# Performance work log

Hardware: AMD Instinct MI355X
Metric: run time of the kernel (lower is better)

The kernel has to match this reference:

```python
import jax, jax.numpy as jnp
import numpy as np

EMB_DIM = 256
Q_DIM = 512
V_DIM = 512

def setup_inputs() -> dict:
    key = jax.random.key(0)
    ks = jax.random.split(key, 7)
    B, S = 8, 2048
    x = jax.random.normal(ks[0], (B, S, EMB_DIM), dtype=jnp.float32)
    s = 1.0 / np.sqrt(EMB_DIM)
    Wq = jax.random.normal(ks[1], (EMB_DIM, Q_DIM), dtype=jnp.float32) * s
    bq = jax.random.normal(ks[2], (Q_DIM,), dtype=jnp.float32) * 0.01
    Wk = jax.random.normal(ks[3], (EMB_DIM, Q_DIM), dtype=jnp.float32) * s
    bk = jax.random.normal(ks[4], (Q_DIM,), dtype=jnp.float32) * 0.01
    Wv = jax.random.normal(ks[5], (EMB_DIM, V_DIM), dtype=jnp.float32) * s
    bv = jax.random.normal(ks[6], (V_DIM,), dtype=jnp.float32) * 0.01
    return {"x": x, "Wq": Wq, "bq": bq, "Wk": Wk, "bk": bk, "Wv": Wv, "bv": bv}

def reference(x, Wq, bq, Wk, bk, Wv, bv):
    # q/k/v projections (torch Linear == x @ W + b with W stored [in, out] here)
    q = jax.nn.sigmoid(jnp.einsum('bse,eq->bsq', x, Wq) + bq)   # [B,S,Q]
    k = jnp.einsum('bse,eq->bsq', x, Wk) + bk                   # [B,S,Q]
    v = jnp.einsum('bse,ev->bsv', x, Wv) + bv                   # [B,S,V]
    scale = 1.0 / jnp.sqrt(jnp.float32(EMB_DIM))
    qk = jnp.einsum('bsq,btq->bst', q, k) * scale               # [B,S,S]
    qk = jax.nn.elu(qk)
    attn = jax.nn.softmax(qk, axis=-1)
    return jnp.einsum('bst,btv->bsv', attn, v)                  # [B,S,V]
```

## Files before the change

kernel.cpp:

```cpp
#include <hip/hip_runtime.h>
#include <hip/hip_bf16.h>
#include <math.h>

typedef unsigned short u16;
using short8 = __attribute__((ext_vector_type(8))) short;
using f32x4  = __attribute__((ext_vector_type(4))) float;

#define BK 32


__device__ __forceinline__ u16 f2bf(float f) {
  union { float f; unsigned u; } v; v.f = f;
  unsigned r = v.u + 0x7FFFu + ((v.u >> 16) & 1u);
  return (u16)(r >> 16);
}

__device__ __forceinline__ float fexp(float x) { return __expf(x); }

__device__ __forceinline__ void gld16(const void* g, void* l) {
  __builtin_amdgcn_global_load_lds(
      (const __attribute__((address_space(1))) void*)g,
      (__attribute__((address_space(3))) void*)l,
      16, 0, 0);
}


__device__ __forceinline__ void gemm_core64(const u16* __restrict__ Ag,
                                            const u16* __restrict__ Bg,
                                            int K, int lda, int ldb,
                                            u16* As, u16* Bs,
                                            f32x4 acc[4][4], int w, int l) {
  const int wm = (w & 1) << 6, wn = (w >> 1) << 6;
  const int ln = l & 15, lq = l >> 4;
  const int sr0 = w * 16 + (l >> 2);
  const int sr1 = 64 + sr0;
  const int skp = (l & 3) * 8;
  const int skg = ((l & 3) ^ ((l >> 3) & 3)) * 8;
  const int kro = (lq ^ ((ln >> 1) & 3)) * 8;

#pragma unroll
  for (int mt = 0; mt < 4; mt++)
#pragma unroll
    for (int nt = 0; nt < 4; nt++) acc[mt][nt] = (f32x4)0.0f;

  for (int k0 = 0; k0 < K; k0 += 64) {
    __syncthreads();
    gld16(Ag + (size_t)sr0 * lda + k0 + skg, As + sr0 * BK + skp);
    gld16(Ag + (size_t)sr1 * lda + k0 + skg, As + sr1 * BK + skp);
    gld16(Ag + (size_t)sr0 * lda + k0 + 32 + skg, As + 4096 + sr0 * BK + skp);
    gld16(Ag + (size_t)sr1 * lda + k0 + 32 + skg, As + 4096 + sr1 * BK + skp);
    gld16(Bg + (size_t)sr0 * ldb + k0 + skg, Bs + sr0 * BK + skp);
    gld16(Bg + (size_t)sr1 * ldb + k0 + skg, Bs + sr1 * BK + skp);
    gld16(Bg + (size_t)sr0 * ldb + k0 + 32 + skg, Bs + 4096 + sr0 * BK + skp);
    gld16(Bg + (size_t)sr1 * ldb + k0 + 32 + skg, Bs + 4096 + sr1 * BK + skp);
    __syncthreads();
#pragma unroll
    for (int h = 0; h < 2; h++) {
      const u16* Ah = As + h * 4096;
      const u16* Bh = Bs + h * 4096;
      short8 af[4], bf[4];
#pragma unroll
      for (int mt = 0; mt < 4; mt++)
        af[mt] = *(const short8*)(Ah + (wm + mt * 16 + ln) * BK + kro);
#pragma unroll
      for (int nt = 0; nt < 4; nt++)
        bf[nt] = *(const short8*)(Bh + (wn + nt * 16 + ln) * BK + kro);
#pragma unroll
      for (int mt = 0; mt < 4; mt++)
#pragma unroll
        for (int nt = 0; nt < 4; nt++)
          acc[mt][nt] = __builtin_amdgcn_mfma_f32_16x16x32_bf16(
              af[mt], bf[nt], acc[mt][nt], 0, 0, 0);
    }
  }
}


__global__ __launch_bounds__(256) void k_conv(
    const float* __restrict__ x, u16* __restrict__ xb,
    const float* __restrict__ Wq, const float* __restrict__ Wk,
    const float* __restrict__ Wv, const float* __restrict__ bq,
    const float* __restrict__ bk, const float* __restrict__ bv,
    u16* __restrict__ Wt, float* __restrict__ bcat,
    float* __restrict__ lsum) {
  const int bid = blockIdx.x;
  if (bid < 4096) {
    int i = bid * 256 + threadIdx.x;
    float4 v = ((const float4*)x)[i];
    ushort4 o;
    o.x = f2bf(v.x); o.y = f2bf(v.y); o.z = f2bf(v.z); o.w = f2bf(v.w);
    ((ushort4*)xb)[i] = o;
  } else if (bid < 5632) {
    int i = (bid - 4096) * 256 + threadIdx.x;
    int nn = i >> 8, e = i & 255;
    int sel = nn >> 9, c = nn & 511;
    const float* W = (sel == 0) ? Wq : (sel == 1) ? Wk : Wv;
    Wt[i] = f2bf(W[e * 512 + c]);
    if (e == 0) {
      const float* bb = (sel == 0) ? bq : (sel == 1) ? bk : bv;
      bcat[nn] = bb[c];
    }
  } else {
    int i = (bid - 5632) * 256 + threadIdx.x;
    lsum[i] = 0.0f;
  }
}


__global__ __launch_bounds__(256) void k_proj(
    const u16* __restrict__ xb, const u16* __restrict__ Wt,
    const float* __restrict__ bcat, u16* __restrict__ qb,
    u16* __restrict__ kb, u16* __restrict__ vtb) {
  __shared__ __align__(16) u16 As8[8 * 4096];
  __shared__ __align__(16) u16 Bs[2 * 4096];
  const int bm = blockIdx.y * 128;
  const int bnq = blockIdx.x;
  const int tid = threadIdx.x, w = tid >> 6, l = tid & 63;
  const int wm = (w & 1) << 6, wn = (w >> 1) << 6;
  const int ln = l & 15, lq = l >> 4;
  const int sr0 = w * 16 + (l >> 2);
  const int sr1 = 64 + sr0;
  const int skp = (l & 3) * 8;
  const int skg = ((l & 3) ^ ((l >> 3) & 3)) * 8;
  const int kro = (lq ^ ((ln >> 1) & 3)) * 8;

#pragma unroll
  for (int kw = 0; kw < 8; kw++) {
    gld16(xb + (size_t)(bm + sr0) * 256 + kw * 32 + skg,
          As8 + kw * 4096 + sr0 * BK + skp);
    gld16(xb + (size_t)(bm + sr1) * 256 + kw * 32 + skg,
          As8 + kw * 4096 + sr1 * BK + skp);
  }

  const int b = bm >> 11, t0 = bm & 2047;
  const int cb = bnq * 128;

  for (int p = 0; p < 3; p++) {
    const u16* Bg = Wt + (size_t)(p * 512 + cb) * 256;
    f32x4 acc[4][4];
#pragma unroll
    for (int mt = 0; mt < 4; mt++)
#pragma unroll
      for (int nt = 0; nt < 4; nt++) acc[mt][nt] = (f32x4)0.0f;

#pragma unroll
    for (int it2 = 0; it2 < 4; it2++) {
      __syncthreads();
      gld16(Bg + (size_t)sr0 * 256 + it2 * 64 + skg, Bs + sr0 * BK + skp);
      gld16(Bg + (size_t)sr1 * 256 + it2 * 64 + skg, Bs + sr1 * BK + skp);
      gld16(Bg + (size_t)sr0 * 256 + it2 * 64 + 32 + skg,
            Bs + 4096 + sr0 * BK + skp);
      gld16(Bg + (size_t)sr1 * 256 + it2 * 64 + 32 + skg,
            Bs + 4096 + sr1 * BK + skp);
      __syncthreads();
#pragma unroll
      for (int h = 0; h < 2; h++) {
        const u16* Aw = As8 + (it2 * 2 + h) * 4096;
        const u16* Bh = Bs + h * 4096;
        short8 af[4], bf[4];
#pragma unroll
        for (int mt = 0; mt < 4; mt++)
          af[mt] = *(const short8*)(Aw + (wm + mt * 16 + ln) * BK + kro);
#pragma unroll
        for (int nt = 0; nt < 4; nt++)
          bf[nt] = *(const short8*)(Bh + (wn + nt * 16 + ln) * BK + kro);
#pragma unroll
        for (int mt = 0; mt < 4; mt++)
#pragma unroll
          for (int nt = 0; nt < 4; nt++)
            acc[mt][nt] = __builtin_amdgcn_mfma_f32_16x16x32_bf16(
                af[mt], bf[nt], acc[mt][nt], 0, 0, 0);
      }
    }

    if (p < 2) {
      u16* dst = p ? kb : qb;
#pragma unroll
      for (int mt = 0; mt < 4; mt++)
#pragma unroll
        for (int r = 0; r < 4; r++) {
          int row = bm + wm + mt * 16 + lq * 4 + r;
#pragma unroll
          for (int nt = 0; nt < 4; nt++) {
            int col = wn + nt * 16 + ln;
            float v = acc[mt][nt][r] + bcat[p * 512 + cb + col];
            float ov = (p == 0) ? __builtin_amdgcn_rcpf(1.0f + fexp(-v)) : v;
            dst[(size_t)row * 512 + cb + col] = f2bf(ov);
          }
        }
    } else {
      u16* tr = As8;
#pragma unroll
      for (int h = 0; h < 2; h++) {
        __syncthreads();
        if ((w & 1) == h) {
#pragma unroll
          for (int mt = 0; mt < 4; mt++)
#pragma unroll
            for (int nt = 0; nt < 4; nt++) {
              int c = wn + nt * 16 + ln;
              float bias = bcat[1024 + cb + c];
#pragma unroll
              for (int r = 0; r < 4; r++) {
                int lr = mt * 16 + lq * 4 + r;
                tr[c * 68 + lr] = f2bf(acc[mt][nt][r] + bias);
              }
            }
        }
        __syncthreads();
        int c2 = tid >> 1, half = tid & 1;
        size_t dbase = ((size_t)b * 512 + cb + c2) * 2048 + t0 + h * 64 + half * 32;
#pragma unroll
        for (int j = 0; j < 4; j++) {
          ushort4 a0 = *(const ushort4*)&tr[c2 * 68 + half * 32 + j * 8];
          ushort4 a1 = *(const ushort4*)&tr[c2 * 68 + half * 32 + j * 8 + 4];
          *(ushort4*)&vtb[dbase + j * 8] = a0;
          *(ushort4*)&vtb[dbase + j * 8 + 4] = a1;
        }
      }
    }
  }
}


__global__ __launch_bounds__(256, 4) void k_qk(const u16* __restrict__ qb,
                                               const u16* __restrict__ kb,
                                               u16* __restrict__ P,
                                               float* __restrict__ lsum) {
  __shared__ __align__(16) u16 As[2 * 4096];
  __shared__ __align__(16) u16 Bs[2 * 4096];
  const int bid = blockIdx.x;
  const int b = bid & 7, t = bid >> 3;
  const int bm = (t >> 4) * 128, bn = (t & 15) * 128;
  const size_t ob = (size_t)b * 2048 * 512;
  const int tid = threadIdx.x, w = tid >> 6, l = tid & 63;
  f32x4 acc[4][4];
  gemm_core64(qb + ob + (size_t)bm * 512, kb + ob + (size_t)bn * 512,
              512, 512, 512, As, Bs, acc, w, l);

  const int wm = (w & 1) << 6, wn = (w >> 1) << 6;
  const int ln = l & 15, lq = l >> 4;
  const float scale = 0.0625f;
#pragma unroll
  for (int mt = 0; mt < 4; mt++)
#pragma unroll
    for (int r = 0; r < 4; r++) {
      int row = bm + wm + mt * 16 + lq * 4 + r;
      float s = 0.0f;
#pragma unroll
      for (int nt = 0; nt < 4; nt++) {
        int col = bn + wn + nt * 16 + ln;
        float v = acc[mt][nt][r] * scale;
        float e = (v > 0.0f) ? v : (fexp(v) - 1.0f);
        float p = fexp(e);
        P[((size_t)b * 2048 + row) * 2048 + col] = f2bf(p);
        s += p;
      }
#pragma unroll
      for (int o = 1; o < 16; o <<= 1) s += __shfl_xor(s, o);
      if (ln == 0) atomicAdd(&lsum[b * 2048 + row], s);
    }
}


__global__ __launch_bounds__(256, 4) void k_pv(const u16* __restrict__ P,
                                               const u16* __restrict__ vtb,
                                               const float* __restrict__ lsum,
                                               float* __restrict__ out) {
  __shared__ __align__(16) u16 As[2 * 4096];
  __shared__ __align__(16) u16 Bs[2 * 4096];
  const int bid = blockIdx.x;
  const int b = bid & 7, t = bid >> 3;
  const int bm = (t >> 2) * 128, bn = (t & 3) * 128;
  const int tid = threadIdx.x, w = tid >> 6, l = tid & 63;
  f32x4 acc[4][4];
  gemm_core64(P  + (size_t)b * 2048 * 2048 + (size_t)bm * 2048,
              vtb + (size_t)b * 512 * 2048 + (size_t)bn * 2048,
              2048, 2048, 2048, As, Bs, acc, w, l);

  const int wm = (w & 1) << 6, wn = (w >> 1) << 6;
  const int ln = l & 15, lq = l >> 4;
#pragma unroll
  for (int mt = 0; mt < 4; mt++)
#pragma unroll
    for (int r = 0; r < 4; r++) {
      int row = bm + wm + mt * 16 + lq * 4 + r;
      float inv = 1.0f / lsum[b * 2048 + row];
#pragma unroll
      for (int nt = 0; nt < 4; nt++) {
        int col = bn + wn + nt * 16 + ln;
        out[((size_t)b * 2048 + row) * 512 + col] = acc[mt][nt][r] * inv;
      }
    }
}


extern "C" void kernel_launch(void* const* d_in, const int* in_sizes, int n_in,
                              void* d_out, int out_size, void* d_ws, size_t ws_size,
                              hipStream_t stream) {
  const float* x  = (const float*)d_in[0];
  const float* Wq = (const float*)d_in[1];
  const float* bq = (const float*)d_in[2];
  const float* Wk = (const float*)d_in[3];
  const float* bk = (const float*)d_in[4];
  const float* Wv = (const float*)d_in[5];
  const float* bv = (const float*)d_in[6];
  float* out = (float*)d_out;
  char* ws = (char*)d_ws;

  u16*  qb   = (u16*)(ws + 0);
  u16*  kb   = (u16*)(ws + 16777216);
  u16*  vtb  = (u16*)(ws + 33554432);
  float* lsum = (float*)(ws + 50331648);
  u16*  P    = (u16*)(ws + 50397184);
  u16*  xb   = (u16*)(ws + 50397184);
  u16*  Wt   = (u16*)(ws + 58785792);
  float* bcat = (float*)(ws + 59572224);

  k_conv<<<5696, 256, 0, stream>>>(x, xb, Wq, Wk, Wv, bq, bk, bv, Wt, bcat, lsum);
  k_proj<<<dim3(4, 128, 1), 256, 0, stream>>>(xb, Wt, bcat, qb, kb, vtb);
  k_qk<<<2048, 256, 0, stream>>>(qb, kb, P, lsum);
  k_pv<<<512, 256, 0, stream>>>(P, vtb, lsum, out);
}
```

Baseline: 200.5 us.

## Replace synchronous GEMM K-loop with three-slot LDS ring prefetch pipeline

The shared GEMM core used by the QK and PV kernels is rewritten from a load-then-compute loop with two barriers per 64-wide K step into a three-slot ring of 32-wide K windows. Loads for window i+2 are issued via global_load_lds while window i is computed, using vmcnt waits and a single barrier per step. The aim is to overlap global-to-LDS transfer latency with MFMA work. It raises LDS use per block from 32KB to 48KB, which may reduce occupancy, and it adds a dependency on hand-tuned waitcnt counts.

```diff
diff --git a/kernel.cpp b/kernel.cpp
--- a/kernel.cpp
+++ b/kernel.cpp
@@ -25,11 +25,11 @@
 }
 
 
-__device__ __forceinline__ void gemm_core64(const u16* __restrict__ Ag,
-                                            const u16* __restrict__ Bg,
-                                            int K, int lda, int ldb,
-                                            u16* As, u16* Bs,
-                                            f32x4 acc[4][4], int w, int l) {
+__device__ __forceinline__ void gemm_ring3(const u16* __restrict__ Ag,
+                                           const u16* __restrict__ Bg,
+                                           int K, int lda, int ldb,
+                                           u16* As, u16* Bs,
+                                           f32x4 acc[4][4], int w, int l) {
   const int wm = (w & 1) << 6, wn = (w >> 1) << 6;
   const int ln = l & 15, lq = l >> 4;
   const int sr0 = w * 16 + (l >> 2);
@@ -43,35 +43,53 @@
 #pragma unroll
     for (int nt = 0; nt < 4; nt++) acc[mt][nt] = (f32x4)0.0f;
 
-  for (int k0 = 0; k0 < K; k0 += 64) {
-    __syncthreads();
-    gld16(Ag + (size_t)sr0 * lda + k0 + skg, As + sr0 * BK + skp);
-    gld16(Ag + (size_t)sr1 * lda + k0 + skg, As + sr1 * BK + skp);
-    gld16(Ag + (size_t)sr0 * lda + k0 + 32 + skg, As + 4096 + sr0 * BK + skp);
-    gld16(Ag + (size_t)sr1 * lda + k0 + 32 + skg, As + 4096 + sr1 * BK + skp);
-    gld16(Bg + (size_t)sr0 * ldb + k0 + skg, Bs + sr0 * BK + skp);
-    gld16(Bg + (size_t)sr1 * ldb + k0 + skg, Bs + sr1 * BK + skp);
-    gld16(Bg + (size_t)sr0 * ldb + k0 + 32 + skg, Bs + 4096 + sr0 * BK + skp);
-    gld16(Bg + (size_t)sr1 * ldb + k0 + 32 + skg, Bs + 4096 + sr1 * BK + skp);
-    __syncthreads();
-#pragma unroll
-    for (int h = 0; h < 2; h++) {
-      const u16* Ah = As + h * 4096;
-      const u16* Bh = Bs + h * 4096;
-      short8 af[4], bf[4];
-#pragma unroll
-      for (int mt = 0; mt < 4; mt++)
-        af[mt] = *(const short8*)(Ah + (wm + mt * 16 + ln) * BK + kro);
+  auto issue = [&](int win, int slot) {
+    const int k = win * 32;
+    u16* Aw = As + slot * 4096;
+    u16* Bw = Bs + slot * 4096;
+    gld16(Ag + (size_t)sr0 * lda + k + skg, Aw + sr0 * BK + skp);
+    gld16(Ag + (size_t)sr1 * lda + k + skg, Aw + sr1 * BK + skp);
+    gld16(Bg + (size_t)sr0 * ldb + k + skg, Bw + sr0 * BK + skp);
+    gld16(Bg + (size_t)sr1 * ldb + k + skg, Bw + sr1 * BK + skp);
+  };
+
+  const int nw = K >> 5;
+  issue(0, 0);
+  issue(1, 1);
+
+  int slot = 0, nslot = 2;
+  for (int i = 0; i < nw; ++i) {
+    if (i + 2 < nw) {
+      asm volatile("s_waitcnt vmcnt(4)" ::: "memory");
+      __builtin_amdgcn_s_barrier();
+      issue(i + 2, nslot);
+    } else if (i + 1 < nw) {
+      asm volatile("s_waitcnt vmcnt(4)" ::: "memory");
+      __builtin_amdgcn_s_barrier();
+    } else {
+      asm volatile("s_waitcnt vmcnt(0)" ::: "memory");
+      __builtin_amdgcn_s_barrier();
+    }
+    asm volatile("" ::: "memory");
+
+    const u16* Ah = As + slot * 4096;
+    const u16* Bh = Bs + slot * 4096;
+    short8 af[4], bf[4];
+#pragma unroll
+    for (int mt = 0; mt < 4; mt++)
+      af[mt] = *(const short8*)(Ah + (wm + mt * 16 + ln) * BK + kro);
+#pragma unroll
+    for (int nt = 0; nt < 4; nt++)
+      bf[nt] = *(const short8*)(Bh + (wn + nt * 16 + ln) * BK + kro);
+#pragma unroll
+    for (int mt = 0; mt < 4; mt++)
 #pragma unroll
       for (int nt = 0; nt < 4; nt++)
-        bf[nt] = *(const short8*)(Bh + (wn + nt * 16 + ln) * BK + kro);
-#pragma unroll
-      for (int mt = 0; mt < 4; mt++)
-#pragma unroll
-        for (int nt = 0; nt < 4; nt++)
-          acc[mt][nt] = __builtin_amdgcn_mfma_f32_16x16x32_bf16(
-              af[mt], bf[nt], acc[mt][nt], 0, 0, 0);
-    }
+        acc[mt][nt] = __builtin_amdgcn_mfma_f32_16x16x32_bf16(
+            af[mt], bf[nt], acc[mt][nt], 0, 0, 0);
+
+    slot = (slot == 2) ? 0 : slot + 1;
+    nslot = (nslot == 2) ? 0 : nslot + 1;
   }
 }
 
@@ -227,16 +245,16 @@
                                                const u16* __restrict__ kb,
                                                u16* __restrict__ P,
                                                float* __restrict__ lsum) {
-  __shared__ __align__(16) u16 As[2 * 4096];
-  __shared__ __align__(16) u16 Bs[2 * 4096];
+  __shared__ __align__(16) u16 As[3 * 4096];
+  __shared__ __align__(16) u16 Bs[3 * 4096];
   const int bid = blockIdx.x;
   const int b = bid & 7, t = bid >> 3;
   const int bm = (t >> 4) * 128, bn = (t & 15) * 128;
   const size_t ob = (size_t)b * 2048 * 512;
   const int tid = threadIdx.x, w = tid >> 6, l = tid & 63;
   f32x4 acc[4][4];
-  gemm_core64(qb + ob + (size_t)bm * 512, kb + ob + (size_t)bn * 512,
-              512, 512, 512, As, Bs, acc, w, l);
+  gemm_ring3(qb + ob + (size_t)bm * 512, kb + ob + (size_t)bn * 512,
+             512, 512, 512, As, Bs, acc, w, l);
 
   const int wm = (w & 1) << 6, wn = (w >> 1) << 6;
   const int ln = l & 15, lq = l >> 4;
@@ -267,16 +285,16 @@
                                                const u16* __restrict__ vtb,
                                                const float* __restrict__ lsum,
                                                float* __restrict__ out) {
-  __shared__ __align__(16) u16 As[2 * 4096];
-  __shared__ __align__(16) u16 Bs[2 * 4096];
+  __shared__ __align__(16) u16 As[3 * 4096];
+  __shared__ __align__(16) u16 Bs[3 * 4096];
   const int bid = blockIdx.x;
   const int b = bid & 7, t = bid >> 3;
   const int bm = (t >> 2) * 128, bn = (t & 3) * 128;
   const int tid = threadIdx.x, w = tid >> 6, l = tid & 63;
   f32x4 acc[4][4];
-  gemm_core64(P  + (size_t)b * 2048 * 2048 + (size_t)bm * 2048,
-              vtb + (size_t)b * 512 * 2048 + (size_t)bn * 2048,
-              2048, 2048, 2048, As, Bs, acc, w, l);
+  gemm_ring3(P  + (size_t)b * 2048 * 2048 + (size_t)bm * 2048,
+             vtb + (size_t)b * 512 * 2048 + (size_t)bn * 2048,
+             2048, 2048, 2048, As, Bs, acc, w, l);
 
   const int wm = (w & 1) << 6, wn = (w >> 1) << 6;
   const int ln = l & 15, lq = l >> 4;
```

New measurement: 225.1 us. +12.3%, slower.

## Enlarge QK kernel tiles to 256x256 with 4-stage LDS pipeline

Applied to the files above, without the earlier changes.

The QK score kernel moves from 128x128 tiles with 256 threads to 256x256 tiles with 512 threads. Its K loop is now written inline as a four-slot global_load_lds pipeline with XOR-swizzled LDS addresses and explicit vmcnt waits. Larger tiles cut the number of times Q and K are loaded and give each wave more MFMA work per fragment load. In exchange it uses far more LDS (128KB) and more accumulator registers, which lowers occupancy, and the grid shrinks to 512 blocks.

```diff
diff --git a/kernel.cpp b/kernel.cpp
--- a/kernel.cpp
+++ b/kernel.cpp
@@ -223,33 +223,85 @@
 }
 
 
-__global__ __launch_bounds__(256, 4) void k_qk(const u16* __restrict__ qb,
+__global__ __launch_bounds__(512, 2) void k_qk(const u16* __restrict__ qb,
                                                const u16* __restrict__ kb,
                                                u16* __restrict__ P,
                                                float* __restrict__ lsum) {
-  __shared__ __align__(16) u16 As[2 * 4096];
-  __shared__ __align__(16) u16 Bs[2 * 4096];
+  __shared__ __align__(16) u16 As[4 * 8192];
+  __shared__ __align__(16) u16 Bs[4 * 8192];
   const int bid = blockIdx.x;
   const int b = bid & 7, t = bid >> 3;
-  const int bm = (t >> 4) * 128, bn = (t & 15) * 128;
+  const int bm = (t >> 3) * 256, bn = (t & 7) * 256;
   const size_t ob = (size_t)b * 2048 * 512;
-  const int tid = threadIdx.x, w = tid >> 6, l = tid & 63;
-  f32x4 acc[4][4];
-  gemm_core64(qb + ob + (size_t)bm * 512, kb + ob + (size_t)bn * 512,
-              512, 512, 512, As, Bs, acc, w, l);
-
-  const int wm = (w & 1) << 6, wn = (w >> 1) << 6;
+  const u16* Ag = qb + ob + (size_t)bm * 512;
+  const u16* Bg = kb + ob + (size_t)bn * 512;
+  const int tid = threadIdx.x;
+  const int w = tid >> 6, l = tid & 63;
+  const int wm = w & 1, wn = w >> 1;
   const int ln = l & 15, lq = l >> 4;
+  const int srow = tid >> 2;
+  const int skp = (tid & 3) * 8;
+  const int skg = ((tid & 3) ^ ((tid >> 3) & 3)) * 8;
+  const int kro = (lq ^ ((ln >> 1) & 3)) * 8;
+
+  f32x4 acc[8][4];
+#pragma unroll
+  for (int mt = 0; mt < 8; mt++)
+#pragma unroll
+    for (int nt = 0; nt < 4; nt++) acc[mt][nt] = (f32x4)0.0f;
+
+  auto stage = [&](int slot, int k0) {
+    u16* Asl = As + slot * 8192;
+    u16* Bsl = Bs + slot * 8192;
+    gld16(Ag + (size_t)srow * 512 + k0 + skg,         Asl + srow * 32 + skp);
+    gld16(Ag + (size_t)(128 + srow) * 512 + k0 + skg, Asl + 4096 + srow * 32 + skp);
+    gld16(Bg + (size_t)srow * 512 + k0 + skg,         Bsl + srow * 32 + skp);
+    gld16(Bg + (size_t)(128 + srow) * 512 + k0 + skg, Bsl + 4096 + srow * 32 + skp);
+  };
+
+  stage(0, 0); stage(1, 32); stage(2, 64);
+  asm volatile("s_waitcnt vmcnt(8)" ::: "memory");
+  __builtin_amdgcn_s_barrier();
+
+  for (int i = 0; i < 16; ++i) {
+    if (i + 3 < 16) stage((i + 3) & 3, (i + 3) * 32);
+    const u16* Asl = As + (i & 3) * 8192;
+    const u16* Bsl = Bs + (i & 3) * 8192;
+    short8 af[8], bf[4];
+#pragma unroll
+    for (int mt = 0; mt < 8; mt++)
+      af[mt] = *(const short8*)(Asl + wm * 4096 + (mt * 16 + ln) * 32 + kro);
+#pragma unroll
+    for (int nt = 0; nt < 4; nt++) {
+      int rb = wn * 64 + nt * 16 + ln;
+      bf[nt] = *(const short8*)(Bsl + (rb >> 7) * 4096 + (rb & 127) * 32 + kro);
+    }
+#pragma unroll
+    for (int mt = 0; mt < 8; mt++)
+#pragma unroll
+      for (int nt = 0; nt < 4; nt++)
+        acc[mt][nt] = __builtin_amdgcn_mfma_f32_16x16x32_bf16(
+            af[mt], bf[nt], acc[mt][nt], 0, 0, 0);
+    if (i + 3 < 16) {
+      asm volatile("s_waitcnt vmcnt(8)" ::: "memory");
+    } else if (i + 2 < 16) {
+      asm volatile("s_waitcnt vmcnt(4)" ::: "memory");
+    } else if (i + 1 < 16) {
+      asm volatile("s_waitcnt vmcnt(0)" ::: "memory");
+    }
+    __builtin_amdgcn_s_barrier();
+  }
+
   const float scale = 0.0625f;
 #pragma unroll
-  for (int mt = 0; mt < 4; mt++)
+  for (int mt = 0; mt < 8; mt++)
 #pragma unroll
     for (int r = 0; r < 4; r++) {
-      int row = bm + wm + mt * 16 + lq * 4 + r;
+      int row = bm + wm * 128 + mt * 16 + lq * 4 + r;
       float s = 0.0f;
 #pragma unroll
       for (int nt = 0; nt < 4; nt++) {
-        int col = bn + wn + nt * 16 + ln;
+        int col = bn + wn * 64 + nt * 16 + ln;
         float v = acc[mt][nt][r] * scale;
         float e = (v > 0.0f) ? v : (fexp(v) - 1.0f);
         float p = fexp(e);
@@ -319,6 +371,6 @@
 
   k_conv<<<5696, 256, 0, stream>>>(x, xb, Wq, Wk, Wv, bq, bk, bv, Wt, bcat, lsum);
   k_proj<<<dim3(4, 128, 1), 256, 0, stream>>>(xb, Wt, bcat, qb, kb, vtb);
-  k_qk<<<2048, 256, 0, stream>>>(qb, kb, P, lsum);
+  k_qk<<<512, 512, 0, stream>>>(qb, kb, P, lsum);
   k_pv<<<512, 256, 0, stream>>>(P, vtb, lsum, out);
 }
```

After: 210.7 us. 1.05x slower.

## Restructure PV kernel to full-width rows with V fragments read directly from global

Applied to the files above, without the earlier changes.

The PV GEMM now gives each block 64 query rows across all 512 value columns, so every P tile is loaded only once. Previously four column tiles each reloaded the same P rows. Only the P tile is staged in LDS, using an XOR swizzle. Each wave reads its V^T fragments straight from global memory (through cache) into registers and keeps a larger 4x8 accumulator. This halves the grid to 256 blocks and lowers launch bounds to 2 blocks per SIMD, which trades occupancy and V reuse through LDS for less P traffic.

```diff
diff --git a/kernel.cpp b/kernel.cpp
--- a/kernel.cpp
+++ b/kernel.cpp
@@ -263,32 +263,63 @@
 }
 
 
-__global__ __launch_bounds__(256, 4) void k_pv(const u16* __restrict__ P,
+__global__ __launch_bounds__(256, 2) void k_pv(const u16* __restrict__ P,
                                                const u16* __restrict__ vtb,
                                                const float* __restrict__ lsum,
                                                float* __restrict__ out) {
-  __shared__ __align__(16) u16 As[2 * 4096];
-  __shared__ __align__(16) u16 Bs[2 * 4096];
+  __shared__ __align__(16) u16 As[2 * 2048];
   const int bid = blockIdx.x;
   const int b = bid & 7, t = bid >> 3;
-  const int bm = (t >> 2) * 128, bn = (t & 3) * 128;
+  const int bm = t * 64;
   const int tid = threadIdx.x, w = tid >> 6, l = tid & 63;
-  f32x4 acc[4][4];
-  gemm_core64(P  + (size_t)b * 2048 * 2048 + (size_t)bm * 2048,
-              vtb + (size_t)b * 512 * 2048 + (size_t)bn * 2048,
-              2048, 2048, 2048, As, Bs, acc, w, l);
-
-  const int wm = (w & 1) << 6, wn = (w >> 1) << 6;
   const int ln = l & 15, lq = l >> 4;
+  const int srow = tid >> 2;
+  const int skp = (tid & 3) * 8;
+  const int skg = ((tid & 3) ^ ((tid >> 3) & 3)) * 8;
+  const int kro = (lq ^ ((ln >> 1) & 3)) * 8;
+
+  const u16* Ag = P + ((size_t)b * 2048 + bm) * 2048;
+  const u16* Bg = vtb + ((size_t)b * 512 + w * 128) * 2048;
+
+  f32x4 acc[4][8];
 #pragma unroll
   for (int mt = 0; mt < 4; mt++)
 #pragma unroll
+    for (int nt = 0; nt < 8; nt++) acc[mt][nt] = (f32x4)0.0f;
+
+  for (int k0 = 0; k0 < 2048; k0 += 64) {
+    __syncthreads();
+    gld16(Ag + (size_t)srow * 2048 + k0 + skg, As + srow * 32 + skp);
+    gld16(Ag + (size_t)srow * 2048 + k0 + 32 + skg, As + 2048 + srow * 32 + skp);
+    __syncthreads();
+#pragma unroll
+    for (int h = 0; h < 2; h++) {
+      const u16* Ah = As + h * 2048;
+      short8 af[4];
+#pragma unroll
+      for (int mt = 0; mt < 4; mt++)
+        af[mt] = *(const short8*)(Ah + (mt * 16 + ln) * 32 + kro);
+#pragma unroll
+      for (int nt = 0; nt < 8; nt++) {
+        short8 bf = *(const short8*)(Bg + (size_t)(nt * 16 + ln) * 2048 +
+                                     k0 + h * 32 + lq * 8);
+#pragma unroll
+        for (int mt = 0; mt < 4; mt++)
+          acc[mt][nt] = __builtin_amdgcn_mfma_f32_16x16x32_bf16(
+              af[mt], bf, acc[mt][nt], 0, 0, 0);
+      }
+    }
+  }
+
+#pragma unroll
+  for (int mt = 0; mt < 4; mt++)
+#pragma unroll
     for (int r = 0; r < 4; r++) {
-      int row = bm + wm + mt * 16 + lq * 4 + r;
+      int row = bm + mt * 16 + lq * 4 + r;
       float inv = 1.0f / lsum[b * 2048 + row];
 #pragma unroll
-      for (int nt = 0; nt < 4; nt++) {
-        int col = bn + wn + nt * 16 + ln;
+      for (int nt = 0; nt < 8; nt++) {
+        int col = w * 128 + nt * 16 + ln;
         out[((size_t)b * 2048 + row) * 512 + col] = acc[mt][nt][r] * inv;
       }
     }
@@ -320,5 +351,5 @@
   k_conv<<<5696, 256, 0, stream>>>(x, xb, Wq, Wk, Wv, bq, bk, bv, Wt, bcat, lsum);
   k_proj<<<dim3(4, 128, 1), 256, 0, stream>>>(xb, Wt, bcat, qb, kb, vtb);
   k_qk<<<2048, 256, 0, stream>>>(qb, kb, P, lsum);
-  k_pv<<<512, 256, 0, stream>>>(P, vtb, lsum, out);
-}
+  k_pv<<<256, 256, 0, stream>>>(P, vtb, lsum, out);
+}
```

After: 278.9 us. +39.1%, slower.
